# Performance work log

Hardware: AMD Instinct MI355X
Metric: run time of the kernel (lower is better)

## Reference

```python
import jax, jax.numpy as jnp
import numpy as np

T, B, NIN, NOUT, H, NLAYER = 512, 32, 72, 90, 512, 5


def _ln(x, g, b):
    m = jnp.mean(x, -1, keepdims=True)
    v = jnp.var(x, -1, keepdims=True)
    return (x - m) * jax.lax.rsqrt(v + 1e-5) * g + b


def _sru_dir(xt, fp, rp, hw, vf, vr, bf, br):
    # xt/fp/rp/hw: (T, B, H) in scan order; elementwise gated recurrence
    def step(c, inp):
        x_t, f_t, r_t, hw_t = inp
        f = jax.nn.sigmoid(f_t + vf * c + bf)
        r = jax.nn.sigmoid(r_t + vr * c + br)
        c2 = f * c + (1.0 - f) * x_t
        h = r * jnp.tanh(c2) + (1.0 - r) * hw_t
        return c2, h
    c0 = jnp.zeros_like(xt[0])
    cT, hs = jax.lax.scan(step, c0, (xt, fp, rp, hw))
    return hs, cT


def _sru_layer(x, W, v, b, g, be, k):
    # x: (T, B, d_in); W: (d_in, 2*k*H); v,b: (2 dirs, 2 gates, H)
    Tl, Bl = x.shape[0], x.shape[1]
    xn = _ln(x, g, be)
    U = (xn @ W).reshape(Tl, Bl, 2, k, H)
    outs, cs = [], []
    for d in range(2):
        Ud = U[:, :, d]
        if d == 1:
            Ud = jnp.flip(Ud, 0)
        # highway: extra projection when d_in != H (k=4), else raw input (k=3)
        hw = Ud[:, :, 3] if k == 4 else (jnp.flip(x, 0) if d == 1 else x)
        hs, cT = _sru_dir(Ud[:, :, 0], Ud[:, :, 1], Ud[:, :, 2], hw,
                          v[d, 0], v[d, 1], b[d, 0], b[d, 1])
        if d == 1:
            hs = jnp.flip(hs, 0)
        outs.append(hs)
        cs.append(cT)
    return jnp.concatenate(outs, -1), jnp.concatenate(cs, -1)


def setup_inputs() -> dict:
    key = jax.random.key(0)
    ks = jax.random.split(key, 12)
    s1 = 1.0 / np.sqrt(NIN)
    s2 = 1.0 / np.sqrt(2 * H)
    s0 = 1.0 / np.sqrt(H)
    return {
        "x": jax.random.normal(ks[0], (T, B, NIN), jnp.float32),
        "W1": jax.random.normal(ks[1], (NIN, H), jnp.float32) * s1,
        "b1": jnp.zeros((H,), jnp.float32),
        "W2": jax.random.normal(ks[2], (2 * H, NOUT), jnp.float32) * s2,
        "b2": jnp.zeros((NOUT,), jnp.float32),
        # SRU layer 0: input H -> 2 dirs * H, k=3 (highway uses raw input)
        "W0": jax.random.normal(ks[3], (H, 2 * 3 * H), jnp.float32) * s0,
        "v0": jax.random.normal(ks[4], (2, 2, H), jnp.float32) * s0,
        "bb0": jnp.zeros((2, 2, H), jnp.float32),
        "g0": jnp.ones((H,), jnp.float32),
        "be0": jnp.zeros((H,), jnp.float32),
        # SRU layers 1..4: input 2H -> 2 dirs * H, k=4 (projected highway)
        "Ws": jax.random.normal(ks[5], (NLAYER - 1, 2 * H, 2 * 4 * H), jnp.float32) * s2,
        "vs": jax.random.normal(ks[6], (NLAYER - 1, 2, 2, H), jnp.float32) * s0,
        "bbs": jnp.zeros((NLAYER - 1, 2, 2, H), jnp.float32),
        "gs": jnp.ones((NLAYER - 1, 2 * H), jnp.float32),
        "bes": jnp.zeros((NLAYER - 1, 2 * H), jnp.float32),
    }


def reference(x, W1, b1, W2, b2, W0, v0, bb0, g0, be0, Ws, vs, bbs, gs, bes):
    h = jax.nn.relu(x @ W1 + b1)  # (T, B, H); dropout is identity at eval
    states = []
    h, c = _sru_layer(h, W0, v0, bb0, g0, be0, 3)
    states.append(c)
    for i in range(Ws.shape[0]):
        h, c = _sru_layer(h, Ws[i], vs[i], bbs[i], gs[i], bes[i], 4)
        states.append(c)
    out = h @ W2 + b2  # (T, B, NOUT)
    return out, jnp.stack(states)  # h state: (NLAYER, B, 2H)
```

## Files before the change

### kernel.cpp

```cpp
#include <hip/hip_runtime.h>
#include <stdint.h>

#define T_LEN 512
#define BATCH 32
#define NIN   72
#define NOUT  90
#define HDIM  512
#define MROWS (T_LEN*BATCH)

typedef unsigned short u16;
typedef unsigned int   u32;

typedef __bf16 bf16x8 __attribute__((ext_vector_type(8)));
typedef short  s16x8  __attribute__((ext_vector_type(8)));
typedef float  f32x4  __attribute__((ext_vector_type(4)));

__device__ __forceinline__ float b2f(u16 u){ return __uint_as_float(((u32)u)<<16); }
__device__ __forceinline__ u16 f2b(float x){
  u32 u = __float_as_uint(x);
  u += 0x7FFFu + ((u>>16)&1u);
  return (u16)(u>>16);
}
__device__ __forceinline__ float sigmoidf_(float z){ return 1.f/(1.f+__expf(-z)); }
__device__ __forceinline__ float tanhf_(float z){ return 2.f/(1.f+__expf(-2.f*z)) - 1.f; }

__device__ __forceinline__ void gload16(const void* g, void* l){
  __builtin_amdgcn_global_load_lds(
      (const __attribute__((address_space(1))) void*)g,
      (__attribute__((address_space(3))) void*)l, 16, 0, 0);
}

__global__ __launch_bounds__(256) void k_transpose_cast(
    const float* __restrict__ S, u16* __restrict__ D, int K, int N, int ldd)
{
  __shared__ float t[32][33];
  int k0 = blockIdx.y*32, n0 = blockIdx.x*32;
  int tx = threadIdx.x, ty = threadIdx.y;
  #pragma unroll
  for (int i=0;i<4;++i){
    int k = k0 + ty + i*8, n = n0 + tx;
    if (k < K && n < N) t[ty+i*8][tx] = S[(size_t)k*N + n];
  }
  __syncthreads();
  #pragma unroll
  for (int i=0;i<4;++i){
    int n = n0 + ty + i*8, k = k0 + tx;
    if (n < N && k < K) D[(size_t)n*ldd + k] = f2b(t[tx][ty+i*8]);
  }
}

__global__ __launch_bounds__(256) void k_gemm1_relu(
    const float* __restrict__ X, const float* __restrict__ W1,
    const float* __restrict__ b1, u16* __restrict__ H0)
{
  __shared__ float As[64][73];
  __shared__ float Bs[72][64];
  int m0 = blockIdx.y*64, n0 = blockIdx.x*64;
  int tid = threadIdx.x;
  for (int idx=tid; idx<64*NIN; idx+=256){ int r=idx/NIN, k=idx-r*NIN; As[r][k] = X[(size_t)(m0+r)*NIN + k]; }
  for (int idx=tid; idx<NIN*64; idx+=256){ int k=idx>>6, n=idx&63; Bs[k][n] = W1[(size_t)k*HDIM + n0+n]; }
  __syncthreads();
  int tx = tid & 15, ty = tid >> 4;
  float acc[4][4] = {};
  for (int k=0;k<NIN;++k){
    float a[4], bv[4];
    #pragma unroll
    for (int i=0;i<4;++i) a[i]=As[ty*4+i][k];
    #pragma unroll
    for (int j=0;j<4;++j) bv[j]=Bs[k][tx*4+j];
    #pragma unroll
    for (int i=0;i<4;++i)
      #pragma unroll
      for (int j=0;j<4;++j) acc[i][j] += a[i]*bv[j];
  }
  #pragma unroll
  for (int i=0;i<4;++i){
    int row = m0 + ty*4 + i;
    #pragma unroll
    for (int j=0;j<4;++j){
      int col = n0 + tx*4 + j;
      float v = acc[i][j] + b1[col];
      H0[(size_t)row*HDIM + col] = f2b(v > 0.f ? v : 0.f);
    }
  }
}

template<int D>
__global__ __launch_bounds__(256) void k_ln(
    const u16* __restrict__ X, const float* __restrict__ g,
    const float* __restrict__ be, u16* __restrict__ Y)
{
  int wrow = (blockIdx.x*256 + threadIdx.x) >> 6;
  int lane = threadIdx.x & 63;
  constexpr int E = D/64;
  const u16* row = X + (size_t)wrow*D;
  float vals[E];
  float s=0.f, s2=0.f;
  #pragma unroll
  for (int i=0;i<E/4;++i){
    ushort4 u = *(const ushort4*)(row + i*256 + lane*4);
    float v0=b2f(u.x), v1=b2f(u.y), v2=b2f(u.z), v3=b2f(u.w);
    vals[i*4+0]=v0; vals[i*4+1]=v1; vals[i*4+2]=v2; vals[i*4+3]=v3;
    s  += v0+v1+v2+v3;
    s2 += v0*v0+v1*v1+v2*v2+v3*v3;
  }
  #pragma unroll
  for (int off=32; off; off>>=1){ s += __shfl_xor(s,off); s2 += __shfl_xor(s2,off); }
  float mean = s * (1.f/D);
  float var  = s2 * (1.f/D) - mean*mean;
  float rstd = rsqrtf(var + 1e-5f);
  u16* yr = Y + (size_t)wrow*D;
  #pragma unroll
  for (int i=0;i<E/4;++i){
    int col = i*256 + lane*4;
    float4 gg = *(const float4*)(g+col);
    float4 bb = *(const float4*)(be+col);
    ushort4 o;
    o.x = f2b((vals[i*4+0]-mean)*rstd*gg.x + bb.x);
    o.y = f2b((vals[i*4+1]-mean)*rstd*gg.y + bb.y);
    o.z = f2b((vals[i*4+2]-mean)*rstd*gg.z + bb.z);
    o.w = f2b((vals[i*4+3]-mean)*rstd*gg.w + bb.w);
    *(ushort4*)(yr + col) = o;
  }
}

__global__ __launch_bounds__(512, 2) void k_gemm256(
    const u16* __restrict__ A, const u16* __restrict__ BT,
    u16* __restrict__ C, int K, int N)
{
  __shared__ u16 lds[65536];
  const int tid  = threadIdx.x;
  const int lane = tid & 63;
  const int wid  = tid >> 6;
  const int wm   = wid >> 2;
  const int wn   = wid & 3;

  const int nbx = gridDim.x;
  const int nwg = nbx * gridDim.y;
  const int bid = blockIdx.y * nbx + blockIdx.x;
  const int cpx = nwg >> 3;
  const int swz = (bid & 7) * cpx + (bid >> 3);
  const int m0 = (swz / nbx) * 256;
  const int n0 = (swz % nbx) * 256;

  const int l3 = lane >> 3, l7 = lane & 7;
  const int kswz = (l7 ^ l3) * 8;

  auto stageA = [&](int ts, int h, int db){
    const u16* base = A + (size_t)(m0 + h*128 + wid*8 + l3)*K + ts*64 + kswz;
    u16* dst = lds + db*32768 + h*8192 + wid*512;
    gload16(base,               dst);
    gload16(base + (size_t)64*K, dst + 4096);
  };
  auto stageB = [&](int ts, int db){
    const u16* base = BT + (size_t)(n0 + wid*8 + l3)*K + ts*64 + kswz;
    u16* dst = lds + db*32768 + 16384 + wid*512;
    gload16(base,                dst);
    gload16(base + (size_t) 64*K, dst + 4096);
    gload16(base + (size_t)128*K, dst + 8192);
    gload16(base + (size_t)192*K, dst + 12288);
  };
  auto rdfrag = [&](const u16* buf, int row, int ks)->bf16x8 {
    int byte = (row*128 + (ks*32 + ((lane>>4)*8))*2) ^ ((row&7)<<4);
    return __builtin_bit_cast(bf16x8, *(const s16x8*)((const char*)buf + byte));
  };

  f32x4 acc[8][4] = {};
  bf16x8 afr[2][2][2];
  bf16x8 bfr0[4][2], bfr1[4][2];
  const int nt = K >> 6;

  stageA(0, 0, 0);
  stageA(0, 1, 0);
  stageB(0, 0);
  asm volatile("s_waitcnt vmcnt(0)" ::: "memory");
  __builtin_amdgcn_sched_barrier(0);
  __builtin_amdgcn_s_barrier();
  __builtin_amdgcn_sched_barrier(0);
  #pragma unroll
  for (int n=0;n<4;++n)
    #pragma unroll
    for (int ks=0;ks<2;++ks)
      bfr0[n][ks] = rdfrag(lds + 16384, wn*64 + n*16 + (lane&15), ks);
  #pragma unroll
  for (int mm=0;mm<2;++mm)
    #pragma unroll
    for (int ks=0;ks<2;++ks)
      afr[0][mm][ks] = rdfrag(lds, wm*128 + mm*16 + (lane&15), ks);

  auto tile = [&](int t, bf16x8 (&bcur)[4][2], bf16x8 (&bnxt)[4][2]){
    const u16* bufA  = lds + (t & 1)*32768;
    const int  tn    = (t+1 < nt) ? t+1 : t;
    const int  db    = (t+1) & 1;
    const u16* bufAn = lds + db*32768;
    const u16* bufBn = bufAn + 16384;

    stageA(tn, 0, db);
    stageA(tn, 1, db);
    stageB(tn, db);

    #pragma unroll
    for (int q=0;q<3;++q){
      asm volatile("s_waitcnt lgkmcnt(0)" ::: "memory");
      __builtin_amdgcn_sched_barrier(0);
      #pragma unroll
      for (int mm=0;mm<2;++mm)
        #pragma unroll
        for (int ks=0;ks<2;++ks)
          afr[(q+1)&1][mm][ks] = rdfrag(bufA, wm*128 + ((q+1)*2+mm)*16 + (lane&15), ks);
      __builtin_amdgcn_sched_barrier(0);
      __builtin_amdgcn_s_setprio(1);
      #pragma unroll
      for (int mm=0;mm<2;++mm)
        #pragma unroll
        for (int n=0;n<4;++n)
          #pragma unroll
          for (int ks=0;ks<2;++ks)
            acc[q*2+mm][n] = __builtin_amdgcn_mfma_f32_16x16x32_bf16(
                afr[q&1][mm][ks], bcur[n][ks], acc[q*2+mm][n], 0,0,0);
      __builtin_amdgcn_s_setprio(0);
    }

    asm volatile("s_waitcnt vmcnt(0) lgkmcnt(0)" ::: "memory");
    __builtin_amdgcn_sched_barrier(0);
    __builtin_amdgcn_s_barrier();
    __builtin_amdgcn_sched_barrier(0);
    #pragma unroll
    for (int mm=0;mm<2;++mm)
      #pragma unroll
      for (int ks=0;ks<2;++ks)
        afr[0][mm][ks] = rdfrag(bufAn, wm*128 + mm*16 + (lane&15), ks);
    #pragma unroll
    for (int n=0;n<4;++n)
      #pragma unroll
      for (int ks=0;ks<2;++ks)
        bnxt[n][ks] = rdfrag(bufBn, wn*64 + n*16 + (lane&15), ks);
    __builtin_amdgcn_sched_barrier(0);
    __builtin_amdgcn_s_setprio(1);
    #pragma unroll
    for (int mm=0;mm<2;++mm)
      #pragma unroll
      for (int n=0;n<4;++n)
        #pragma unroll
        for (int ks=0;ks<2;++ks)
          acc[6+mm][n] = __builtin_amdgcn_mfma_f32_16x16x32_bf16(
              afr[1][mm][ks], bcur[n][ks], acc[6+mm][n], 0,0,0);
    __builtin_amdgcn_s_setprio(0);
  };

  for (int t = 0; t < nt; t += 2){
    tile(t,   bfr0, bfr1);
    tile(t+1, bfr1, bfr0);
  }

  #pragma unroll
  for (int m=0;m<8;++m){
    int row = m0 + wm*128 + m*16 + ((lane>>4)<<2);
    #pragma unroll
    for (int n=0;n<4;++n){
      int col = n0 + wn*64 + n*16 + (lane&15);
      #pragma unroll
      for (int i=0;i<4;++i)
        C[(size_t)(row+i)*N + col] = f2b(acc[m][n][i]);
    }
  }
}

template<bool OUT_F32, bool HAS_BIAS>
__global__ __launch_bounds__(256) void k_gemm(
    const u16* __restrict__ A, const u16* __restrict__ BT,
    void* __restrict__ Cv, const float* __restrict__ bias,
    int K, int N, int ldc, int nbound)
{
  __shared__ u16 As[128*64];
  __shared__ u16 Bs[128*64];
  const int tid  = threadIdx.x;
  const int lane = tid & 63;
  const int wid  = tid >> 6;

  const int nbx = gridDim.x;
  const int nwg = nbx * gridDim.y;
  const int bid = blockIdx.y * nbx + blockIdx.x;
  const int cpx = nwg >> 3;
  const int swzb = (bid & 7) * cpx + (bid >> 3);
  const int bx = swzb % nbx, by = swzb / nbx;

  const int m0 = by * 128;
  const int n0 = bx * 128;
  const int wr = wid >> 1, wc = wid & 1;
  f32x4 acc[4][4] = {};

  const int srow = lane >> 3;
  const int skel = (lane & 7) * 8;

  for (int kt = 0; kt < K; kt += 64) {
    #pragma unroll
    for (int i=0;i<4;++i){
      int seg  = wid*4 + i;
      int arow = seg*8 + srow;
      gload16(A  + (size_t)(m0 + arow)*K + kt + skel, As + seg*512);
      gload16(BT + (size_t)(n0 + arow)*K + kt + skel, Bs + seg*512);
    }
    __syncthreads();
    #pragma unroll
    for (int ks=0; ks<2; ++ks){
      bf16x8 a[4], b[4];
      #pragma unroll
      for (int m=0;m<4;++m){
        int off = (wr*64 + m*16 + (lane&15))*64 + ks*32 + (lane>>4)*8;
        a[m] = __builtin_bit_cast(bf16x8, *(const s16x8*)(As + off));
      }
      #pragma unroll
      for (int n=0;n<4;++n){
        int off = (wc*64 + n*16 + (lane&15))*64 + ks*32 + (lane>>4)*8;
        b[n] = __builtin_bit_cast(bf16x8, *(const s16x8*)(Bs + off));
      }
      #pragma unroll
      for (int m=0;m<4;++m)
        #pragma unroll
        for (int n=0;n<4;++n)
          acc[m][n] = __builtin_amdgcn_mfma_f32_16x16x32_bf16(a[m], b[n], acc[m][n], 0,0,0);
    }
    __syncthreads();
  }

  #pragma unroll
  for (int m=0;m<4;++m){
    #pragma unroll
    for (int n=0;n<4;++n){
      int col = n0 + wc*64 + n*16 + (lane & 15);
      #pragma unroll
      for (int i=0;i<4;++i){
        int row = m0 + wr*64 + m*16 + ((lane>>4)<<2) + i;
        float v = acc[m][n][i];
        if (OUT_F32) {
          if (col < nbound){
            float bv = HAS_BIAS ? bias[col] : 0.f;
            ((float*)Cv)[(size_t)row*ldc + col] = v + bv;
          }
        } else {
          ((u16*)Cv)[(size_t)row*ldc + col] = f2b(v);
        }
      }
    }
  }
}

template<int KG>
__global__ __launch_bounds__(64) void k_scan(
    const u16* __restrict__ U, const u16* __restrict__ hwsrc,
    const float* __restrict__ v, const float* __restrict__ bb,
    u16* __restrict__ hout, float* __restrict__ states)
{
  constexpr int NS = 16;
  constexpr int D  = 14;
  constexpr int NITER = T_LEN/2;
  __shared__ u16 ring[NS*512];

  const int lane = threadIdx.x;
  const int bid  = blockIdx.x;
  const int hblk = bid & 7;
  const int b    = (bid >> 3) & 31;
  const int d    = bid >> 8;
  const int h    = hblk*64 + lane;
  const int RS   = 2*KG*HDIM;

  const int s2 = lane >> 5, p = (lane>>3)&3, c7 = lane&7;

  auto issue = [&](int k, int slot){
    int s = 2*k + s2;
    int t = d ? (T_LEN-1-s) : s;
    int row = t*BATCH + b;
    const u16* g;
    if (KG == 4 || p < 3)
      g = U + (size_t)row*RS + (size_t)(d*KG + p)*HDIM + hblk*64 + c7*8;
    else
      g = hwsrc + (size_t)row*HDIM + hblk*64 + c7*8;
    gload16(g, &ring[slot*512]);
  };

  for (int k=0;k<D;++k) issue(k, k);
  asm volatile("s_waitcnt vmcnt(0)" ::: "memory");
  __builtin_amdgcn_sched_barrier(0);

  const float vf  = v[(d*2+0)*HDIM + h];
  const float vr  = v[(d*2+1)*HDIM + h];
  const float bf_ = bb[(d*2+0)*HDIM + h];
  const float br_ = bb[(d*2+1)*HDIM + h];

  float cst = 0.f;
  for (int k=0;k<NITER;++k){
    int kk = (k+D < NITER) ? (k+D) : (NITER-1);
    issue(kk, (k+D) & (NS-1));
    asm volatile("s_waitcnt vmcnt(42)" ::: "memory");
    __builtin_amdgcn_sched_barrier(0);

    const int slot = k & (NS-1);
    #pragma unroll
    for (int j=0;j<2;++j){
      int s = 2*k + j;
      int t = d ? (T_LEN-1-s) : s;
      const u16* base = ring + slot*512 + j*256;
      float xv = b2f(base[0*64 + lane]);
      float fv = b2f(base[1*64 + lane]);
      float rv = b2f(base[2*64 + lane]);
      float wv = b2f(base[3*64 + lane]);
      float f = sigmoidf_(fv + vf*cst + bf_);
      float r = sigmoidf_(rv + vr*cst + br_);
      cst = f*cst + (1.f-f)*xv;
      float hv = r*tanhf_(cst) + (1.f-r)*wv;
      hout[(size_t)(t*BATCH + b)*(2*HDIM) + d*HDIM + h] = f2b(hv);
    }
  }
  states[(size_t)b*(2*HDIM) + d*HDIM + h] = cst;
}

extern "C" void kernel_launch(void* const* d_in, const int* in_sizes, int n_in,
                              void* d_out, int out_size, void* d_ws, size_t ws_size,
                              hipStream_t stream)
{
  const float* x   = (const float*)d_in[0];
  const float* W1  = (const float*)d_in[1];
  const float* b1  = (const float*)d_in[2];
  const float* W2  = (const float*)d_in[3];
  const float* b2  = (const float*)d_in[4];
  const float* W0  = (const float*)d_in[5];
  const float* v0  = (const float*)d_in[6];
  const float* bb0 = (const float*)d_in[7];
  const float* g0  = (const float*)d_in[8];
  const float* be0 = (const float*)d_in[9];
  const float* Ws  = (const float*)d_in[10];
  const float* vs  = (const float*)d_in[11];
  const float* bbs = (const float*)d_in[12];
  const float* gs  = (const float*)d_in[13];
  const float* bes = (const float*)d_in[14];
  (void)in_sizes; (void)n_in; (void)out_size; (void)ws_size;

  char* ws = (char*)d_ws;
  size_t off = 0;
  auto alloc = [&](size_t bytes)->void*{
    void* p = ws + off; off += (bytes + 255) & ~(size_t)255; return p;
  };
  u16* W0T  = (u16*)alloc((size_t)3072*512*2);
  u16* WsT  = (u16*)alloc((size_t)4*4096*1024*2);
  u16* W2T  = (u16*)alloc((size_t)128*1024*2);
  u16* h0   = (u16*)alloc((size_t)MROWS*512*2);
  u16* xn   = (u16*)alloc((size_t)MROWS*1024*2);
  u16* Ubuf = (u16*)alloc((size_t)MROWS*4096*2);
  u16* hbuf = (u16*)alloc((size_t)MROWS*1024*2);

  float* outp   = (float*)d_out;
  float* states = outp + (size_t)MROWS*NOUT;

  hipMemsetAsync(W2T, 0, (size_t)128*1024*2, stream);
  k_transpose_cast<<<dim3(3072/32, 512/32), dim3(32,8), 0, stream>>>(W0, W0T, 512, 3072, 512);
  for (int i=0;i<4;++i)
    k_transpose_cast<<<dim3(4096/32, 1024/32), dim3(32,8), 0, stream>>>(
        Ws + (size_t)i*1024*4096, WsT + (size_t)i*4096*1024, 1024, 4096, 1024);
  k_transpose_cast<<<dim3(3, 1024/32), dim3(32,8), 0, stream>>>(W2, W2T, 1024, NOUT, 1024);

  k_gemm1_relu<<<dim3(HDIM/64, MROWS/64), 256, 0, stream>>>(x, W1, b1, h0);

  k_ln<512><<<MROWS/4, 256, 0, stream>>>(h0, g0, be0, xn);
  k_gemm256<<<dim3(3072/256, MROWS/256), 512, 0, stream>>>(xn, W0T, Ubuf, 512, 3072);
  k_scan<3><<<512, 64, 0, stream>>>(Ubuf, h0, v0, bb0, hbuf, states);

  for (int i=0;i<4;++i){
    k_ln<1024><<<MROWS/4, 256, 0, stream>>>(hbuf, gs + (size_t)i*1024, bes + (size_t)i*1024, xn);
    k_gemm256<<<dim3(4096/256, MROWS/256), 512, 0, stream>>>(
        xn, WsT + (size_t)i*4096*1024, Ubuf, 1024, 4096);
    k_scan<4><<<512, 64, 0, stream>>>(Ubuf, nullptr, vs + (size_t)i*2048, bbs + (size_t)i*2048,
                                      hbuf, states + (size_t)(i+1)*BATCH*1024);
  }

  k_gemm<true,true><<<dim3(1, MROWS/128), 256, 0, stream>>>(
      hbuf, W2T, d_out, b2, 1024, 128, NOUT, NOUT);
}
```

Before: 1.267 ms.

## Load GEMM B fragments directly from global into registers, halving LDS footprint

The 256x256 bf16 GEMM no longer stages the B tile through shared memory. Each wave now loads its B fragments straight from global memory into registers for the next k-step, while A stays double-buffered in LDS with a new 32-row-per-wave staging pattern. The LDS allocation is halved, and the end-of-tile wait leaves the B loads in flight so they overlap the A barrier. This removes the LDS write/read round-trip for B and may let two workgroups share a CU. The cost is less coalesced global reads for B and duplicated B loads across the two wave rows that share the same columns.

Result: slower. 1.458 ms (+15.1%).

```diff
diff --git a/kernel.cpp b/kernel.cpp
--- a/kernel.cpp
+++ b/kernel.cpp
@@ -128,7 +128,7 @@
     const u16* __restrict__ A, const u16* __restrict__ BT,
     u16* __restrict__ C, int K, int N)
 {
-  __shared__ u16 lds[65536];
+  __shared__ u16 lds[32768];
   const int tid  = threadIdx.x;
   const int lane = tid & 63;
   const int wid  = tid >> 6;
@@ -146,21 +146,23 @@
   const int l3 = lane >> 3, l7 = lane & 7;
   const int kswz = (l7 ^ l3) * 8;
 
-  auto stageA = [&](int ts, int h, int db){
-    const u16* base = A + (size_t)(m0 + h*128 + wid*8 + l3)*K + ts*64 + kswz;
-    u16* dst = lds + db*32768 + h*8192 + wid*512;
-    gload16(base,               dst);
-    gload16(base + (size_t)64*K, dst + 4096);
-  };
-  auto stageB = [&](int ts, int db){
-    const u16* base = BT + (size_t)(n0 + wid*8 + l3)*K + ts*64 + kswz;
-    u16* dst = lds + db*32768 + 16384 + wid*512;
+  auto stageA = [&](int ts, int db){
+    const u16* base = A + (size_t)(m0 + wid*32 + l3)*K + ts*64 + kswz;
+    u16* dst = lds + db*16384 + wid*2048;
     gload16(base,                dst);
-    gload16(base + (size_t) 64*K, dst + 4096);
-    gload16(base + (size_t)128*K, dst + 8192);
-    gload16(base + (size_t)192*K, dst + 12288);
-  };
-  auto rdfrag = [&](const u16* buf, int row, int ks)->bf16x8 {
+    gload16(base + (size_t) 8*K, dst + 512);
+    gload16(base + (size_t)16*K, dst + 1024);
+    gload16(base + (size_t)24*K, dst + 1536);
+  };
+  auto loadB = [&](int ts, bf16x8 (&dst)[4][2]){
+    #pragma unroll
+    for (int n=0;n<4;++n)
+      #pragma unroll
+      for (int ks=0;ks<2;++ks)
+        dst[n][ks] = __builtin_bit_cast(bf16x8, *(const s16x8*)(
+            BT + (size_t)(n0 + wn*64 + n*16 + (lane&15))*K + ts*64 + ks*32 + (lane>>4)*8));
+  };
+  auto rdA = [&](const u16* buf, int row, int ks)->bf16x8 {
     int byte = (row*128 + (ks*32 + ((lane>>4)*8))*2) ^ ((row&7)<<4);
     return __builtin_bit_cast(bf16x8, *(const s16x8*)((const char*)buf + byte));
   };
@@ -170,44 +172,35 @@
   bf16x8 bfr0[4][2], bfr1[4][2];
   const int nt = K >> 6;
 
-  stageA(0, 0, 0);
-  stageA(0, 1, 0);
-  stageB(0, 0);
+  stageA(0, 0);
+  loadB(0, bfr0);
   asm volatile("s_waitcnt vmcnt(0)" ::: "memory");
   __builtin_amdgcn_sched_barrier(0);
   __builtin_amdgcn_s_barrier();
   __builtin_amdgcn_sched_barrier(0);
   #pragma unroll
-  for (int n=0;n<4;++n)
+  for (int mm=0;mm<2;++mm)
     #pragma unroll
     for (int ks=0;ks<2;++ks)
-      bfr0[n][ks] = rdfrag(lds + 16384, wn*64 + n*16 + (lane&15), ks);
-  #pragma unroll
-  for (int mm=0;mm<2;++mm)
-    #pragma unroll
-    for (int ks=0;ks<2;++ks)
-      afr[0][mm][ks] = rdfrag(lds, wm*128 + mm*16 + (lane&15), ks);
+      afr[0][mm][ks] = rdA(lds, wm*128 + mm*16 + (lane&15), ks);
 
   auto tile = [&](int t, bf16x8 (&bcur)[4][2], bf16x8 (&bnxt)[4][2]){
-    const u16* bufA  = lds + (t & 1)*32768;
+    const u16* bufA  = lds + (t & 1)*16384;
     const int  tn    = (t+1 < nt) ? t+1 : t;
     const int  db    = (t+1) & 1;
-    const u16* bufAn = lds + db*32768;
-    const u16* bufBn = bufAn + 16384;
-
-    stageA(tn, 0, db);
-    stageA(tn, 1, db);
-    stageB(tn, db);
+    const u16* bufAn = lds + db*16384;
+
+    stageA(tn, db);
+    loadB(tn, bnxt);
+    __builtin_amdgcn_sched_barrier(0);
 
     #pragma unroll
     for (int q=0;q<3;++q){
-      asm volatile("s_waitcnt lgkmcnt(0)" ::: "memory");
-      __builtin_amdgcn_sched_barrier(0);
       #pragma unroll
       for (int mm=0;mm<2;++mm)
         #pragma unroll
         for (int ks=0;ks<2;++ks)
-          afr[(q+1)&1][mm][ks] = rdfrag(bufA, wm*128 + ((q+1)*2+mm)*16 + (lane&15), ks);
+          afr[(q+1)&1][mm][ks] = rdA(bufA, wm*128 + ((q+1)*2+mm)*16 + (lane&15), ks);
       __builtin_amdgcn_sched_barrier(0);
       __builtin_amdgcn_s_setprio(1);
       #pragma unroll
@@ -221,7 +214,7 @@
       __builtin_amdgcn_s_setprio(0);
     }
 
-    asm volatile("s_waitcnt vmcnt(0) lgkmcnt(0)" ::: "memory");
+    asm volatile("s_waitcnt vmcnt(8) lgkmcnt(0)" ::: "memory");
     __builtin_amdgcn_sched_barrier(0);
     __builtin_amdgcn_s_barrier();
     __builtin_amdgcn_sched_barrier(0);
@@ -229,12 +222,7 @@
     for (int mm=0;mm<2;++mm)
       #pragma unroll
       for (int ks=0;ks<2;++ks)
-        afr[0][mm][ks] = rdfrag(bufAn, wm*128 + mm*16 + (lane&15), ks);
-    #pragma unroll
-    for (int n=0;n<4;++n)
-      #pragma unroll
-      for (int ks=0;ks<2;++ks)
-        bnxt[n][ks] = rdfrag(bufBn, wn*64 + n*16 + (lane&15), ks);
+        afr[0][mm][ks] = rdA(bufAn, wm*128 + mm*16 + (lane&15), ks);
     __builtin_amdgcn_sched_barrier(0);
     __builtin_amdgcn_s_setprio(1);
     #pragma unroll
```
